# Kernel tuning notes

Measured on AMD Instinct MI355X. Metric: run time of the kernel, lower is better.

The kernel has to match this reference:

```python
import jax, jax.numpy as jnp
import numpy as np

N_NODES = 50000
N_EDGES = 800000
INPUT_DIM = 8
HIDDEN_DIM = 128


def setup_inputs() -> dict:
    key = jax.random.key(0)
    k = jax.random.split(key, 8)
    x = jax.random.normal(k[0], (N_NODES, INPUT_DIM), dtype=jnp.float32)
    edge_index = jax.random.randint(k[1], (2, N_EDGES), 0, N_NODES, dtype=jnp.int64)
    edge_attr = jax.random.uniform(k[2], (N_EDGES, 1), dtype=jnp.float32)
    node_embedding = jax.random.normal(k[3], (N_NODES, HIDDEN_DIM), dtype=jnp.float32)
    # Linear weights stored as [in, out] so y = x @ W (bias=False everywhere)
    s1 = 1.0 / np.sqrt(INPUT_DIM)
    sh = 1.0 / np.sqrt(HIDDEN_DIM)
    W1 = jax.random.uniform(k[4], (INPUT_DIM, HIDDEN_DIM), jnp.float32, -s1, s1)
    W2 = jax.random.uniform(k[5], (HIDDEN_DIM, HIDDEN_DIM), jnp.float32, -sh, sh)
    W3 = jax.random.uniform(k[6], (HIDDEN_DIM, HIDDEN_DIM), jnp.float32, -sh, sh)
    W4 = jax.random.uniform(k[7], (1, HIDDEN_DIM), jnp.float32, -1.0, 1.0)
    return {"x": x, "edge_index": edge_index, "edge_attr": edge_attr,
            "node_embedding": node_embedding, "W1": W1, "W2": W2, "W3": W3, "W4": W4}


def reference(x, edge_index, edge_attr, node_embedding, W1, W2, W3, W4):
    n = x.shape[0]
    row, col = edge_index[0], edge_index[1]
    # theta_1(x): [N, hidden]
    node_feature_embedding = x @ W1
    # gather neighbor embeddings along edges, scatter-sum to destination rows
    node_embedding_aggr = jax.ops.segment_sum(node_embedding[col], row, num_segments=n)
    # relu(theta_4(edge_attr)): [E, hidden], then scatter-sum to rows
    edge_feature_embedding = jax.nn.relu(edge_attr @ W4)
    edge_embedding_aggr = jax.ops.segment_sum(edge_feature_embedding, row, num_segments=n)
    return jax.nn.relu(node_feature_embedding + node_embedding_aggr @ W2 + edge_embedding_aggr @ W3)
```

## Files before the change

### kernel.cpp

```cpp
#include <hip/hip_runtime.h>

#define N_NODES 50000
#define N_EDGES 800000
#define IN_DIM  8
#define HD      128
#define N_SCAN_BLOCKS ((N_NODES + 255) / 256)
#define NREP 8
#define NTILES ((N_NODES + 63) / 64)

typedef unsigned short ushort_t;
typedef __attribute__((ext_vector_type(8))) short short8;
typedef __attribute__((ext_vector_type(4))) float float4v;

static __device__ inline unsigned short f2bf(float f) {
    unsigned u = __float_as_uint(f);
    unsigned r = (u + 0x7FFF + ((u >> 16) & 1)) >> 16;
    return (unsigned short)r;
}
static __device__ inline float bf2f(unsigned short b) {
    return __uint_as_float(((unsigned)b) << 16);
}

__global__ void v3_kernel(const float* __restrict__ W4,
                          const float* __restrict__ W3,
                          float* __restrict__ v3) {
    int j = threadIdx.x;
    float acc = 0.f;
    for (int k = 0; k < HD; ++k) {
        float w = W4[k];
        w = w > 0.f ? w : 0.f;
        acc += w * W3[k * HD + j];
    }
    v3[j] = acc;
}

__global__ __launch_bounds__(256, 2)
void gemm_T_mfma(const float* __restrict__ emb,
                 const float* __restrict__ W2,
                 ushort_t* __restrict__ T16) {
    __shared__ short8 bshare[32][64];
    int wave = threadIdx.x >> 6;
    int lane = threadIdx.x & 63;
    int n16  = lane & 15;
    int quad = lane >> 4;

#pragma unroll
    for (int i = 0; i < 8; ++i) {
        int f  = wave * 8 + i;
        int ct = f >> 2, ki = f & 3;
        short8 fr;
#pragma unroll
        for (int j = 0; j < 8; ++j) {
            int k = ki * 32 + quad * 8 + j;
            fr[j] = (short)f2bf(W2[k * HD + ct * 16 + n16]);
        }
        bshare[f][lane] = fr;
    }
    __syncthreads();

    short8 bfrag[8][4];
#pragma unroll
    for (int ct = 0; ct < 8; ++ct)
#pragma unroll
        for (int ki = 0; ki < 4; ++ki)
            bfrag[ct][ki] = bshare[ct * 4 + ki][lane];

    for (int tt = blockIdx.x; tt < NTILES; tt += gridDim.x) {
        int rowbase = tt * 64 + wave * 16;
        int row  = rowbase + n16;
        int rowc = row < N_NODES ? row : N_NODES - 1;
        const float4* arow = (const float4*)(emb + (size_t)rowc * HD);

        short8 afrag[4];
#pragma unroll
        for (int ki = 0; ki < 4; ++ki) {
            float4 lo = arow[ki * 8 + quad * 2];
            float4 hi = arow[ki * 8 + quad * 2 + 1];
            short8 a;
            a[0] = (short)f2bf(lo.x); a[1] = (short)f2bf(lo.y);
            a[2] = (short)f2bf(lo.z); a[3] = (short)f2bf(lo.w);
            a[4] = (short)f2bf(hi.x); a[5] = (short)f2bf(hi.y);
            a[6] = (short)f2bf(hi.z); a[7] = (short)f2bf(hi.w);
            afrag[ki] = a;
        }

        float4v acc[8];
#pragma unroll
        for (int ct = 0; ct < 8; ++ct) acc[ct] = (float4v){0.f, 0.f, 0.f, 0.f};

#pragma unroll
        for (int ki = 0; ki < 4; ++ki)
#pragma unroll
            for (int ct = 0; ct < 8; ++ct)
                acc[ct] = __builtin_amdgcn_mfma_f32_16x16x32_bf16(
                    afrag[ki], bfrag[ct][ki], acc[ct], 0, 0, 0);

#pragma unroll
        for (int reg = 0; reg < 4; ++reg) {
            int r = rowbase + quad * 4 + reg;
            if (r < N_NODES) {
#pragma unroll
                for (int ct = 0; ct < 8; ++ct)
                    T16[(size_t)r * HD + ct * 16 + n16] = f2bf(acc[ct][reg]);
            }
        }
    }
}

__global__ void hist_kernel(const int* __restrict__ ei,
                            int* __restrict__ cnt,
                            ushort_t* __restrict__ rank16) {
    int e = blockIdx.x * 256 + threadIdx.x;
    int rep = blockIdx.x & (NREP - 1);
    int r = ei[e];
    int rank = atomicAdd(&cnt[rep * N_NODES + r], 1);
    rank16[e] = (ushort_t)rank;
}

__global__ void scan1_kernel(const int* __restrict__ cnt,
                             int* __restrict__ off,
                             int* __restrict__ bases,
                             int* __restrict__ blocksums) {
    __shared__ int lds[256];
    int t = threadIdx.x;
    int n = blockIdx.x * 256 + t;
    int c[NREP];
    int tsum = 0;
#pragma unroll
    for (int r = 0; r < NREP; ++r) {
        c[r] = (n < N_NODES) ? cnt[r * N_NODES + n] : 0;
        tsum += c[r];
    }
    lds[t] = tsum;
    __syncthreads();
    for (int o = 1; o < 256; o <<= 1) {
        int add = (t >= o) ? lds[t - o] : 0;
        __syncthreads();
        lds[t] += add;
        __syncthreads();
    }
    int ex = lds[t] - tsum;
    if (n < N_NODES) {
        off[n] = ex;
        int run = ex;
#pragma unroll
        for (int r = 0; r < NREP; ++r) {
            bases[r * N_NODES + n] = run;
            run += c[r];
        }
    }
    if (t == 255) blocksums[blockIdx.x] = lds[255];
}

__global__ void scan2_kernel(int* __restrict__ blocksums,
                             int* __restrict__ off) {
    __shared__ int lds[256];
    int t = threadIdx.x;
    int v = (t < N_SCAN_BLOCKS) ? blocksums[t] : 0;
    lds[t] = v;
    __syncthreads();
    for (int o = 1; o < 256; o <<= 1) {
        int add = (t >= o) ? lds[t - o] : 0;
        __syncthreads();
        lds[t] += add;
        __syncthreads();
    }
    if (t < N_SCAN_BLOCKS) blocksums[t] = lds[t] - v;
    if (t == 255) off[N_NODES] = lds[255];
}

__global__ void scan3_kernel(int* __restrict__ off,
                             int* __restrict__ bases,
                             const int* __restrict__ blocksums) {
    int t = threadIdx.x;
    int n = blockIdx.x * 256 + t;
    if (n >= N_NODES) return;
    int add = blocksums[blockIdx.x];
    off[n] += add;
#pragma unroll
    for (int r = 0; r < NREP; ++r)
        bases[r * N_NODES + n] += add;
}

__global__ void fill_kernel(const int* __restrict__ ei,
                            const float* __restrict__ attr,
                            const ushort_t* __restrict__ rank16,
                            const int* __restrict__ bases,
                            int2* __restrict__ col_attr) {
    int e = blockIdx.x * 256 + threadIdx.x;
    int rep = (e >> 8) & (NREP - 1);
    int r = ei[e];
    int pos = bases[rep * N_NODES + r] + (int)rank16[e];
    int2 p;
    p.x = ei[N_EDGES + e];
    p.y = __float_as_int(attr[e]);
    col_attr[pos] = p;
}

__global__ void aggregate_kernel(const int* __restrict__ off,
                                 const int2* __restrict__ col_attr,
                                 const ushort_t* __restrict__ T16,
                                 const float* __restrict__ x,
                                 const float* __restrict__ W1,
                                 const float* __restrict__ v3,
                                 float* __restrict__ out) {
    int tid  = blockIdx.x * 256 + threadIdx.x;
    int node = tid >> 5;
    int lane = tid & 31;
    int s   = off[node];
    int deg = off[node + 1] - s;
    float4 acc = make_float4(0.f, 0.f, 0.f, 0.f);
    float ssum = 0.f;

    for (int base = 0; base < deg; base += 32) {
        int rem = deg - base; if (rem > 32) rem = 32;
        int2 p = make_int2(0, 0);
        if (lane < rem) p = col_attr[s + base + lane];
        ssum += __int_as_float(p.y);
        int j = 0;
        for (; j + 4 <= rem; j += 4) {
            int c0 = __shfl(p.x, j + 0, 32);
            int c1 = __shfl(p.x, j + 1, 32);
            int c2 = __shfl(p.x, j + 2, 32);
            int c3 = __shfl(p.x, j + 3, 32);
            ushort4 t0 = ((const ushort4*)(T16 + (size_t)c0 * HD))[lane];
            ushort4 t1 = ((const ushort4*)(T16 + (size_t)c1 * HD))[lane];
            ushort4 t2 = ((const ushort4*)(T16 + (size_t)c2 * HD))[lane];
            ushort4 t3 = ((const ushort4*)(T16 + (size_t)c3 * HD))[lane];
            acc.x += (bf2f(t0.x) + bf2f(t1.x)) + (bf2f(t2.x) + bf2f(t3.x));
            acc.y += (bf2f(t0.y) + bf2f(t1.y)) + (bf2f(t2.y) + bf2f(t3.y));
            acc.z += (bf2f(t0.z) + bf2f(t1.z)) + (bf2f(t2.z) + bf2f(t3.z));
            acc.w += (bf2f(t0.w) + bf2f(t1.w)) + (bf2f(t2.w) + bf2f(t3.w));
        }
        for (; j < rem; ++j) {
            int c = __shfl(p.x, j, 32);
            ushort4 t = ((const ushort4*)(T16 + (size_t)c * HD))[lane];
            acc.x += bf2f(t.x);
            acc.y += bf2f(t.y);
            acc.z += bf2f(t.z);
            acc.w += bf2f(t.w);
        }
    }
    for (int o = 16; o; o >>= 1) ssum += __shfl_xor(ssum, o, 32);

    float4 b = ((const float4*)v3)[lane];
    acc.x += ssum * b.x; acc.y += ssum * b.y;
    acc.z += ssum * b.z; acc.w += ssum * b.w;
#pragma unroll
    for (int i = 0; i < IN_DIM; ++i) {
        float xi = x[node * IN_DIM + i];
        float4 w = ((const float4*)(W1 + i * HD))[lane];
        acc.x += xi * w.x; acc.y += xi * w.y;
        acc.z += xi * w.z; acc.w += xi * w.w;
    }
    acc.x = fmaxf(acc.x, 0.f);
    acc.y = fmaxf(acc.y, 0.f);
    acc.z = fmaxf(acc.z, 0.f);
    acc.w = fmaxf(acc.w, 0.f);
    ((float4*)(out + (size_t)node * HD))[lane] = acc;
}

extern "C" void kernel_launch(void* const* d_in, const int* in_sizes, int n_in,
                              void* d_out, int out_size, void* d_ws, size_t ws_size,
                              hipStream_t stream) {
    const float* x    = (const float*)d_in[0];
    const int*   ei   = (const int*)  d_in[1];
    const float* attr = (const float*)d_in[2];
    const float* emb  = (const float*)d_in[3];
    const float* W1   = (const float*)d_in[4];
    const float* W2   = (const float*)d_in[5];
    const float* W3   = (const float*)d_in[6];
    const float* W4   = (const float*)d_in[7];
    float* out = (float*)d_out;

    char* w = (char*)d_ws;
    int2*     col_attr = (int2*)w;
    ushort_t* T16      = (ushort_t*)(w + (size_t)N_EDGES * 8);
    int*      off      = (int*)(w + (size_t)N_EDGES * 8 + (size_t)N_NODES * HD * 2);
    int*      bases    = off + N_NODES + 1;
    int*      cnt      = bases + NREP * N_NODES;
    int*      bsums    = cnt + NREP * N_NODES;
    float*    v3       = (float*)(bsums + 256);
    ushort_t* rank16   = (ushort_t*)(v3 + HD);

    hipMemsetAsync(cnt, 0, (size_t)NREP * N_NODES * sizeof(int), stream);

    v3_kernel   <<<1, HD, 0, stream>>>(W4, W3, v3);
    gemm_T_mfma <<<391, 256, 0, stream>>>(emb, W2, T16);
    hist_kernel <<<N_EDGES / 256, 256, 0, stream>>>(ei, cnt, rank16);
    scan1_kernel<<<N_SCAN_BLOCKS, 256, 0, stream>>>(cnt, off, bases, bsums);
    scan2_kernel<<<1, 256, 0, stream>>>(bsums, off);
    scan3_kernel<<<N_SCAN_BLOCKS, 256, 0, stream>>>(off, bases, bsums);
    fill_kernel <<<N_EDGES / 256, 256, 0, stream>>>(ei, attr, rank16, bases, col_attr);
    aggregate_kernel<<<(N_NODES * 32) / 256, 256, 0, stream>>>(
        off, col_attr, T16, x, W1, v3, out);
}
```

Baseline: 205.5 us.

## Fuse GEMM with histogram, drop scan3, pack edges, widen aggregate lanes

Several changes land together. W2 fragments are precomputed once by a prep kernel. The MFMA GEMM and the edge histogram now run in one interleaved launch. scan3 is removed by adding block sums lazily in the fill and aggregate kernels, and v3 is folded into the scan2 launch. Edges are packed into 32-bit words (16-bit column plus bf16 attribute). The aggregate uses 16 lanes per node with 16-byte gathers, and NREP is raised to 16 to reduce atomic contention. This trades fewer launches and less memory traffic for a lossy bf16 edge attribute, and it relies on node indices fitting in 16 bits.

```diff
diff --git a/kernel.cpp b/kernel.cpp
--- a/kernel.cpp
+++ b/kernel.cpp
@@ -5,10 +5,13 @@
 #define IN_DIM  8
 #define HD      128
 #define N_SCAN_BLOCKS ((N_NODES + 255) / 256)
-#define NREP 8
+#define NREP 16
 #define NTILES ((N_NODES + 63) / 64)
+#define N_HIST_BLOCKS (N_EDGES / 256)
+#define GRID_P1 (NTILES * 5)
 
 typedef unsigned short ushort_t;
+typedef unsigned int uint_t;
 typedef __attribute__((ext_vector_type(8))) short short8;
 typedef __attribute__((ext_vector_type(4))) float float4v;
 
@@ -21,41 +24,57 @@
     return __uint_as_float(((unsigned)b) << 16);
 }
 
-__global__ void v3_kernel(const float* __restrict__ W4,
-                          const float* __restrict__ W3,
-                          float* __restrict__ v3) {
-    int j = threadIdx.x;
-    float acc = 0.f;
-    for (int k = 0; k < HD; ++k) {
-        float w = W4[k];
-        w = w > 0.f ? w : 0.f;
-        acc += w * W3[k * HD + j];
-    }
-    v3[j] = acc;
-}
-
-__global__ __launch_bounds__(256, 2)
-void gemm_T_mfma(const float* __restrict__ emb,
-                 const float* __restrict__ W2,
-                 ushort_t* __restrict__ T16) {
-    __shared__ short8 bshare[32][64];
-    int wave = threadIdx.x >> 6;
-    int lane = threadIdx.x & 63;
-    int n16  = lane & 15;
-    int quad = lane >> 4;
-
+__global__ void prep_kernel(const float* __restrict__ W2,
+                            short8* __restrict__ blob) {
+    int t = threadIdx.x;
 #pragma unroll
     for (int i = 0; i < 8; ++i) {
-        int f  = wave * 8 + i;
+        int slot = t * 8 + i;
+        int f    = slot >> 6;
+        int lane = slot & 63;
         int ct = f >> 2, ki = f & 3;
+        int n16 = lane & 15, quad = lane >> 4;
         short8 fr;
 #pragma unroll
         for (int j = 0; j < 8; ++j) {
             int k = ki * 32 + quad * 8 + j;
             fr[j] = (short)f2bf(W2[k * HD + ct * 16 + n16]);
         }
-        bshare[f][lane] = fr;
-    }
+        blob[slot] = fr;
+    }
+}
+
+__global__ __launch_bounds__(256, 2)
+void phase1_kernel(const float* __restrict__ emb,
+                   const short8* __restrict__ blob,
+                   ushort_t* __restrict__ T16,
+                   const int* __restrict__ ei,
+                   int* __restrict__ cnt,
+                   ushort_t* __restrict__ rank16) {
+    __shared__ short8 sblob[2048];
+    int sel = blockIdx.x % 5;
+
+    if (sel != 0) {
+        int c = (blockIdx.x / 5) * 4 + sel - 1;
+        if (c >= N_HIST_BLOCKS) return;
+        int e = c * 256 + threadIdx.x;
+        int rep = c & (NREP - 1);
+        int r = ei[e];
+        int rank = atomicAdd(&cnt[rep * N_NODES + r], 1);
+        rank16[e] = (ushort_t)rank;
+        return;
+    }
+
+    int tt   = blockIdx.x / 5;
+    int t    = threadIdx.x;
+    int wave = t >> 6;
+    int lane = t & 63;
+    int n16  = lane & 15;
+    int quad = lane >> 4;
+
+#pragma unroll
+    for (int i = 0; i < 8; ++i)
+        sblob[t * 8 + i] = blob[t * 8 + i];
     __syncthreads();
 
     short8 bfrag[8][4];
@@ -63,58 +82,46 @@
     for (int ct = 0; ct < 8; ++ct)
 #pragma unroll
         for (int ki = 0; ki < 4; ++ki)
-            bfrag[ct][ki] = bshare[ct * 4 + ki][lane];
-
-    for (int tt = blockIdx.x; tt < NTILES; tt += gridDim.x) {
-        int rowbase = tt * 64 + wave * 16;
-        int row  = rowbase + n16;
-        int rowc = row < N_NODES ? row : N_NODES - 1;
-        const float4* arow = (const float4*)(emb + (size_t)rowc * HD);
-
-        short8 afrag[4];
-#pragma unroll
-        for (int ki = 0; ki < 4; ++ki) {
-            float4 lo = arow[ki * 8 + quad * 2];
-            float4 hi = arow[ki * 8 + quad * 2 + 1];
-            short8 a;
-            a[0] = (short)f2bf(lo.x); a[1] = (short)f2bf(lo.y);
-            a[2] = (short)f2bf(lo.z); a[3] = (short)f2bf(lo.w);
-            a[4] = (short)f2bf(hi.x); a[5] = (short)f2bf(hi.y);
-            a[6] = (short)f2bf(hi.z); a[7] = (short)f2bf(hi.w);
-            afrag[ki] = a;
-        }
-
-        float4v acc[8];
-#pragma unroll
-        for (int ct = 0; ct < 8; ++ct) acc[ct] = (float4v){0.f, 0.f, 0.f, 0.f};
-
-#pragma unroll
-        for (int ki = 0; ki < 4; ++ki)
+            bfrag[ct][ki] = sblob[(ct * 4 + ki) * 64 + lane];
+
+    int rowbase = tt * 64 + wave * 16;
+    int row  = rowbase + n16;
+    int rowc = row < N_NODES ? row : N_NODES - 1;
+    const float4* arow = (const float4*)(emb + (size_t)rowc * HD);
+
+    short8 afrag[4];
+#pragma unroll
+    for (int ki = 0; ki < 4; ++ki) {
+        float4 lo = arow[ki * 8 + quad * 2];
+        float4 hi = arow[ki * 8 + quad * 2 + 1];
+        short8 a;
+        a[0] = (short)f2bf(lo.x); a[1] = (short)f2bf(lo.y);
+        a[2] = (short)f2bf(lo.z); a[3] = (short)f2bf(lo.w);
+        a[4] = (short)f2bf(hi.x); a[5] = (short)f2bf(hi.y);
+        a[6] = (short)f2bf(hi.z); a[7] = (short)f2bf(hi.w);
+        afrag[ki] = a;
+    }
+
+    float4v acc[8];
+#pragma unroll
+    for (int ct = 0; ct < 8; ++ct) acc[ct] = (float4v){0.f, 0.f, 0.f, 0.f};
+
+#pragma unroll
+    for (int ki = 0; ki < 4; ++ki)
+#pragma unroll
+        for (int ct = 0; ct < 8; ++ct)
+            acc[ct] = __builtin_amdgcn_mfma_f32_16x16x32_bf16(
+                afrag[ki], bfrag[ct][ki], acc[ct], 0, 0, 0);
+
+#pragma unroll
+    for (int reg = 0; reg < 4; ++reg) {
+        int r = rowbase + quad * 4 + reg;
+        if (r < N_NODES) {
 #pragma unroll
             for (int ct = 0; ct < 8; ++ct)
-                acc[ct] = __builtin_amdgcn_mfma_f32_16x16x32_bf16(
-                    afrag[ki], bfrag[ct][ki], acc[ct], 0, 0, 0);
-
-#pragma unroll
-        for (int reg = 0; reg < 4; ++reg) {
-            int r = rowbase + quad * 4 + reg;
-            if (r < N_NODES) {
-#pragma unroll
-                for (int ct = 0; ct < 8; ++ct)
-                    T16[(size_t)r * HD + ct * 16 + n16] = f2bf(acc[ct][reg]);
-            }
-        }
-    }
-}
-
-__global__ void hist_kernel(const int* __restrict__ ei,
-                            int* __restrict__ cnt,
-                            ushort_t* __restrict__ rank16) {
-    int e = blockIdx.x * 256 + threadIdx.x;
-    int rep = blockIdx.x & (NREP - 1);
-    int r = ei[e];
-    int rank = atomicAdd(&cnt[rep * N_NODES + r], 1);
-    rank16[e] = (ushort_t)rank;
+                T16[(size_t)r * HD + ct * 16 + n16] = f2bf(acc[ct][reg]);
+        }
+    }
 }
 
 __global__ void scan1_kernel(const int* __restrict__ cnt,
@@ -152,10 +159,24 @@
     if (t == 255) blocksums[blockIdx.x] = lds[255];
 }
 
-__global__ void scan2_kernel(int* __restrict__ blocksums,
-                             int* __restrict__ off) {
+__global__ void scan2_v3_kernel(int* __restrict__ blocksums,
+                                const float* __restrict__ W4,
+                                const float* __restrict__ W3,
+                                float* __restrict__ v3) {
+    int t = threadIdx.x;
+    if (blockIdx.x == 1) {
+        if (t < HD) {
+            float acc = 0.f;
+            for (int k = 0; k < HD; ++k) {
+                float w = W4[k];
+                w = w > 0.f ? w : 0.f;
+                acc += w * W3[k * HD + t];
+            }
+            v3[t] = acc;
+        }
+        return;
+    }
     __shared__ int lds[256];
-    int t = threadIdx.x;
     int v = (t < N_SCAN_BLOCKS) ? blocksums[t] : 0;
     lds[t] = v;
     __syncthreads();
@@ -166,98 +187,98 @@
         __syncthreads();
     }
     if (t < N_SCAN_BLOCKS) blocksums[t] = lds[t] - v;
-    if (t == 255) off[N_NODES] = lds[255];
-}
-
-__global__ void scan3_kernel(int* __restrict__ off,
-                             int* __restrict__ bases,
-                             const int* __restrict__ blocksums) {
-    int t = threadIdx.x;
-    int n = blockIdx.x * 256 + t;
-    if (n >= N_NODES) return;
-    int add = blocksums[blockIdx.x];
-    off[n] += add;
-#pragma unroll
-    for (int r = 0; r < NREP; ++r)
-        bases[r * N_NODES + n] += add;
 }
 
 __global__ void fill_kernel(const int* __restrict__ ei,
                             const float* __restrict__ attr,
                             const ushort_t* __restrict__ rank16,
                             const int* __restrict__ bases,
-                            int2* __restrict__ col_attr) {
+                            const int* __restrict__ bsums,
+                            uint_t* __restrict__ packed) {
     int e = blockIdx.x * 256 + threadIdx.x;
     int rep = (e >> 8) & (NREP - 1);
     int r = ei[e];
-    int pos = bases[rep * N_NODES + r] + (int)rank16[e];
-    int2 p;
-    p.x = ei[N_EDGES + e];
-    p.y = __float_as_int(attr[e]);
-    col_attr[pos] = p;
+    int pos = bases[rep * N_NODES + r] + bsums[r >> 8] + (int)rank16[e];
+    uint_t p = ((uint_t)f2bf(attr[e]) << 16) | (uint_t)ei[N_EDGES + e];
+    packed[pos] = p;
 }
 
 __global__ void aggregate_kernel(const int* __restrict__ off,
-                                 const int2* __restrict__ col_attr,
+                                 const int* __restrict__ bsums,
+                                 const uint_t* __restrict__ packed,
                                  const ushort_t* __restrict__ T16,
                                  const float* __restrict__ x,
                                  const float* __restrict__ W1,
                                  const float* __restrict__ v3,
                                  float* __restrict__ out) {
     int tid  = blockIdx.x * 256 + threadIdx.x;
-    int node = tid >> 5;
-    int lane = tid & 31;
-    int s   = off[node];
-    int deg = off[node + 1] - s;
-    float4 acc = make_float4(0.f, 0.f, 0.f, 0.f);
+    int node = tid >> 4;
+    int lane = tid & 15;
+    int s  = off[node] + bsums[node >> 8];
+    int e1 = (node + 1 == N_NODES) ? N_EDGES
+                                   : off[node + 1] + bsums[(node + 1) >> 8];
+    int deg = e1 - s;
+
+    float acc[8];
+#pragma unroll
+    for (int i = 0; i < 8; ++i) acc[i] = 0.f;
     float ssum = 0.f;
 
-    for (int base = 0; base < deg; base += 32) {
-        int rem = deg - base; if (rem > 32) rem = 32;
-        int2 p = make_int2(0, 0);
-        if (lane < rem) p = col_attr[s + base + lane];
-        ssum += __int_as_float(p.y);
+    for (int base = 0; base < deg; base += 16) {
+        int rem = deg - base; if (rem > 16) rem = 16;
+        uint_t p = 0;
+        if (lane < rem) p = packed[s + base + lane];
+        ssum += __uint_as_float(p & 0xFFFF0000u);
+        int col = (int)(p & 0xFFFFu);
         int j = 0;
         for (; j + 4 <= rem; j += 4) {
-            int c0 = __shfl(p.x, j + 0, 32);
-            int c1 = __shfl(p.x, j + 1, 32);
-            int c2 = __shfl(p.x, j + 2, 32);
-            int c3 = __shfl(p.x, j + 3, 32);
-            ushort4 t0 = ((const ushort4*)(T16 + (size_t)c0 * HD))[lane];
-            ushort4 t1 = ((const ushort4*)(T16 + (size_t)c1 * HD))[lane];
-            ushort4 t2 = ((const ushort4*)(T16 + (size_t)c2 * HD))[lane];
-            ushort4 t3 = ((const ushort4*)(T16 + (size_t)c3 * HD))[lane];
-            acc.x += (bf2f(t0.x) + bf2f(t1.x)) + (bf2f(t2.x) + bf2f(t3.x));
-            acc.y += (bf2f(t0.y) + bf2f(t1.y)) + (bf2f(t2.y) + bf2f(t3.y));
-            acc.z += (bf2f(t0.z) + bf2f(t1.z)) + (bf2f(t2.z) + bf2f(t3.z));
-            acc.w += (bf2f(t0.w) + bf2f(t1.w)) + (bf2f(t2.w) + bf2f(t3.w));
+            int c0 = __shfl(col, j + 0, 16);
+            int c1 = __shfl(col, j + 1, 16);
+            int c2 = __shfl(col, j + 2, 16);
+            int c3 = __shfl(col, j + 3, 16);
+            short8 t0 = ((const short8*)(T16 + (size_t)c0 * HD))[lane];
+            short8 t1 = ((const short8*)(T16 + (size_t)c1 * HD))[lane];
+            short8 t2 = ((const short8*)(T16 + (size_t)c2 * HD))[lane];
+            short8 t3 = ((const short8*)(T16 + (size_t)c3 * HD))[lane];
+#pragma unroll
+            for (int i = 0; i < 8; ++i)
+                acc[i] += (bf2f((ushort_t)t0[i]) + bf2f((ushort_t)t1[i]))
+                        + (bf2f((ushort_t)t2[i]) + bf2f((ushort_t)t3[i]));
         }
         for (; j < rem; ++j) {
-            int c = __shfl(p.x, j, 32);
-            ushort4 t = ((const ushort4*)(T16 + (size_t)c * HD))[lane];
-            acc.x += bf2f(t.x);
-            acc.y += bf2f(t.y);
-            acc.z += bf2f(t.z);
-            acc.w += bf2f(t.w);
-        }
-    }
-    for (int o = 16; o; o >>= 1) ssum += __shfl_xor(ssum, o, 32);
-
-    float4 b = ((const float4*)v3)[lane];
-    acc.x += ssum * b.x; acc.y += ssum * b.y;
-    acc.z += ssum * b.z; acc.w += ssum * b.w;
+            int c = __shfl(col, j, 16);
+            short8 tv = ((const short8*)(T16 + (size_t)c * HD))[lane];
+#pragma unroll
+            for (int i = 0; i < 8; ++i)
+                acc[i] += bf2f((ushort_t)tv[i]);
+        }
+    }
+    for (int o = 8; o; o >>= 1) ssum += __shfl_xor(ssum, o, 16);
+
+    const float4* v3p = (const float4*)v3;
+    float4 b0 = v3p[lane * 2], b1 = v3p[lane * 2 + 1];
+    acc[0] += ssum * b0.x; acc[1] += ssum * b0.y;
+    acc[2] += ssum * b0.z; acc[3] += ssum * b0.w;
+    acc[4] += ssum * b1.x; acc[5] += ssum * b1.y;
+    acc[6] += ssum * b1.z; acc[7] += ssum * b1.w;
 #pragma unroll
     for (int i = 0; i < IN_DIM; ++i) {
         float xi = x[node * IN_DIM + i];
-        float4 w = ((const float4*)(W1 + i * HD))[lane];
-        acc.x += xi * w.x; acc.y += xi * w.y;
-        acc.z += xi * w.z; acc.w += xi * w.w;
-    }
-    acc.x = fmaxf(acc.x, 0.f);
-    acc.y = fmaxf(acc.y, 0.f);
-    acc.z = fmaxf(acc.z, 0.f);
-    acc.w = fmaxf(acc.w, 0.f);
-    ((float4*)(out + (size_t)node * HD))[lane] = acc;
+        const float4* wp = (const float4*)(W1 + i * HD);
+        float4 w0 = wp[lane * 2], w1 = wp[lane * 2 + 1];
+        acc[0] += xi * w0.x; acc[1] += xi * w0.y;
+        acc[2] += xi * w0.z; acc[3] += xi * w0.w;
+        acc[4] += xi * w1.x; acc[5] += xi * w1.y;
+        acc[6] += xi * w1.z; acc[7] += xi * w1.w;
+    }
+    float4 o0, o1;
+    o0.x = fmaxf(acc[0], 0.f); o0.y = fmaxf(acc[1], 0.f);
+    o0.z = fmaxf(acc[2], 0.f); o0.w = fmaxf(acc[3], 0.f);
+    o1.x = fmaxf(acc[4], 0.f); o1.y = fmaxf(acc[5], 0.f);
+    o1.z = fmaxf(acc[6], 0.f); o1.w = fmaxf(acc[7], 0.f);
+    float4* op = (float4*)(out + (size_t)node * HD);
+    op[lane * 2]     = o0;
+    op[lane * 2 + 1] = o1;
 }
 
 extern "C" void kernel_launch(void* const* d_in, const int* in_sizes, int n_in,
@@ -274,24 +295,23 @@
     float* out = (float*)d_out;
 
     char* w = (char*)d_ws;
-    int2*     col_attr = (int2*)w;
-    ushort_t* T16      = (ushort_t*)(w + (size_t)N_EDGES * 8);
-    int*      off      = (int*)(w + (size_t)N_EDGES * 8 + (size_t)N_NODES * HD * 2);
-    int*      bases    = off + N_NODES + 1;
-    int*      cnt      = bases + NREP * N_NODES;
-    int*      bsums    = cnt + NREP * N_NODES;
-    float*    v3       = (float*)(bsums + 256);
-    ushort_t* rank16   = (ushort_t*)(v3 + HD);
+    uint_t*   packed = (uint_t*)w;
+    ushort_t* T16    = (ushort_t*)(w + (size_t)N_EDGES * 4);
+    short8*   blob   = (short8*)((char*)T16 + (size_t)N_NODES * HD * 2);
+    int*      off    = (int*)((char*)blob + 2048 * 16);
+    int*      bases  = off + N_NODES + 4;
+    int*      cnt    = bases + NREP * N_NODES;
+    int*      bsums  = cnt + NREP * N_NODES;
+    float*    v3     = (float*)(bsums + 256);
+    ushort_t* rank16 = (ushort_t*)(v3 + HD);
 
     hipMemsetAsync(cnt, 0, (size_t)NREP * N_NODES * sizeof(int), stream);
 
-    v3_kernel   <<<1, HD, 0, stream>>>(W4, W3, v3);
-    gemm_T_mfma <<<391, 256, 0, stream>>>(emb, W2, T16);
-    hist_kernel <<<N_EDGES / 256, 256, 0, stream>>>(ei, cnt, rank16);
-    scan1_kernel<<<N_SCAN_BLOCKS, 256, 0, stream>>>(cnt, off, bases, bsums);
-    scan2_kernel<<<1, 256, 0, stream>>>(bsums, off);
-    scan3_kernel<<<N_SCAN_BLOCKS, 256, 0, stream>>>(off, bases, bsums);
-    fill_kernel <<<N_EDGES / 256, 256, 0, stream>>>(ei, attr, rank16, bases, col_attr);
-    aggregate_kernel<<<(N_NODES * 32) / 256, 256, 0, stream>>>(
-        off, col_attr, T16, x, W1, v3, out);
-}
+    prep_kernel  <<<1, 256, 0, stream>>>(W2, blob);
+    phase1_kernel<<<GRID_P1, 256, 0, stream>>>(emb, blob, T16, ei, cnt, rank16);
+    scan1_kernel <<<N_SCAN_BLOCKS, 256, 0, stream>>>(cnt, off, bases, bsums);
+    scan2_v3_kernel<<<2, 256, 0, stream>>>(bsums, W4, W3, v3);
+    fill_kernel  <<<N_HIST_BLOCKS, 256, 0, stream>>>(ei, attr, rank16, bases, bsums, packed);
+    aggregate_kernel<<<(N_NODES * 16) / 256, 256, 0, stream>>>(
+        off, bsums, packed, T16, x, W1, v3, out);
+}
```

Measured after the change: 188.6 us. 1.09x faster.
